# Optimization experiments

Hardware: AMD Instinct MI355X
Metric: run time of the kernel (lower is better)

Reference implementation:

```python
import jax, jax.numpy as jnp
import numpy as np

EPS = 1e-5

def _layernorm(x, gamma):
    # LayerNorm over last dim, no bias (torch LayerNorm(bias=False))
    mu = jnp.mean(x, axis=-1, keepdims=True)
    var = jnp.mean(jnp.square(x - mu), axis=-1, keepdims=True)
    return (x - mu) * jax.lax.rsqrt(var + EPS) * gamma

def setup_inputs() -> dict:
    B, N, D = 32, 1024, 512
    key = jax.random.key(0)
    ks = jax.random.split(key, 6)
    x = jax.random.normal(ks[0], (B, N, D), dtype=jnp.float32)
    # valid lengths in [1, N] so no query row has all keys masked
    belief_base_sizes = jax.random.randint(ks[1], (B,), 1, N + 1, dtype=jnp.int32)
    s = 0.02
    w_qkv = jax.random.normal(ks[2], (D, 3 * D), dtype=jnp.float32) * s
    w_fc = jax.random.normal(ks[3], (D, D), dtype=jnp.float32) * s
    w_proj = jax.random.normal(ks[4], (D, D), dtype=jnp.float32) * s
    g1 = jnp.ones((D,), dtype=jnp.float32)
    g2 = jnp.ones((D,), dtype=jnp.float32)
    return {"x": x, "belief_base_sizes": belief_base_sizes, "g1": g1,
            "w_qkv": w_qkv, "g2": g2, "w_fc": w_fc, "w_proj": w_proj}

def reference(x, belief_base_sizes, g1, w_qkv, g2, w_fc, w_proj):
    B, N, D = x.shape
    h = _layernorm(x, g1)                      # LN1
    qkv = jnp.einsum('bnd,de->bne', h, w_qkv)  # [B,N,3D]
    q, k, v = jnp.split(qkv, 3, axis=-1)
    scores = jnp.einsum('bqd,bkd->bqk', q, k) / jnp.sqrt(jnp.float32(D))
    # mask key columns >= valid size (rows are NOT masked, matching the original)
    col = jnp.arange(N)
    pad = col[None, None, :] >= belief_base_sizes[:, None, None]  # [B,1,N]
    scores = jnp.where(pad, -jnp.inf, scores)
    attn = jax.nn.softmax(scores, axis=-1)
    y = jnp.einsum('bqk,bkd->bqd', attn, v)
    y = _layernorm(y, g2)                      # LN2 (no residual in original)
    y = jnp.einsum('bnd,de->bne', y, w_fc)
    y = jax.nn.gelu(y, approximate=False)      # torch GELU default = exact erf
    y = jnp.einsum('bnd,de->bne', y, w_proj)
    return y
```

## Files before the change

kernel.cpp:

```cpp
#include <hip/hip_runtime.h>
#include <hip/hip_bf16.h>
#include <cmath>


using f16 = _Float16;
typedef _Float16 f16x8 __attribute__((ext_vector_type(8)));
typedef _Float16 f16x4 __attribute__((ext_vector_type(4)));
typedef _Float16 f16x2 __attribute__((ext_vector_type(2)));
typedef float f32x4 __attribute__((ext_vector_type(4)));

#define NB 32
#define NN 1024
#define ND 512

#define GLOAD_LDS16(g, l)                                                     \
    __builtin_amdgcn_global_load_lds(                                         \
        (const __attribute__((address_space(1))) void*)(g),                   \
        (__attribute__((address_space(3))) void*)(l), 16, 0, 0)

__global__ void transpose_cast_all(const float* __restrict__ wqkv, f16* __restrict__ wqkvT,
                                   const float* __restrict__ wfc, f16* __restrict__ wfcT,
                                   const float* __restrict__ wproj, f16* __restrict__ wprojT) {
    const int z = blockIdx.z;
    const float* w = (z == 0) ? wqkv : (z == 1) ? wfc : wproj;
    f16* wT       = (z == 0) ? wqkvT : (z == 1) ? wfcT : wprojT;
    const int Ncols = (z == 0) ? 1536 : 512;
    if ((int)blockIdx.x * 32 >= Ncols) return;

    __shared__ float tile[32][33];
    const int n0 = blockIdx.x * 32, k0 = blockIdx.y * 32;
    const int tx = threadIdx.x, ty = threadIdx.y;
    for (int i = ty; i < 32; i += 8)
        tile[i][tx] = w[(long long)(k0 + i) * Ncols + n0 + tx];
    __syncthreads();
    for (int i = ty; i < 32; i += 8)
        wT[(long long)(n0 + i) * 512 + k0 + tx] = (f16)tile[tx][i];
}

template <typename TIN>
__global__ __launch_bounds__(256) void ln_kernel(const TIN* __restrict__ x,
                                                 const float* __restrict__ gamma,
                                                 f16* __restrict__ out) {
    const int tid = threadIdx.x;
    const long long base = (long long)blockIdx.x * ND;
    float v0, v1;
    if constexpr (sizeof(TIN) == 4) {
        const float2 t = ((const float2*)(x + base))[tid];
        v0 = t.x; v1 = t.y;
    } else {
        const f16x2 t = ((const f16x2*)(x + base))[tid];
        v0 = (float)t.x; v1 = (float)t.y;
    }

    __shared__ float red[8];
    const int wave = tid >> 6, lane = tid & 63;

    float s = v0 + v1;
#pragma unroll
    for (int o = 32; o > 0; o >>= 1) s += __shfl_down(s, o, 64);
    if (lane == 0) red[wave] = s;
    __syncthreads();
    const float mean = (red[0] + red[1] + red[2] + red[3]) * (1.f / 512.f);
    __syncthreads();

    const float d0 = v0 - mean, d1 = v1 - mean;
    float q = d0 * d0 + d1 * d1;
#pragma unroll
    for (int o = 32; o > 0; o >>= 1) q += __shfl_down(q, o, 64);
    if (lane == 0) red[wave] = q;
    __syncthreads();
    const float var = (red[0] + red[1] + red[2] + red[3]) * (1.f / 512.f);
    const float rstd = rsqrtf(var + 1e-5f);

    f16x2 o2;
    o2.x = (f16)(d0 * rstd * gamma[2 * tid]);
    o2.y = (f16)(d1 * rstd * gamma[2 * tid + 1]);
    ((f16x2*)(out + base))[tid] = o2;
}

__global__ __launch_bounds__(256) void softmax_wave(f16* __restrict__ scores,
                                                    const int* __restrict__ sizes) {
    const int b = blockIdx.y;
    const int wave = threadIdx.x >> 6, lane = threadIdx.x & 63;
    const int row = blockIdx.x * 4 + wave;
    f16* srow = scores + ((long long)b * NN + row) * NN;
    const int sz = sizes[b];
    const int keff = (sz + 63) & ~63;
    const int cbase = lane * 16;

    float v[16];
    if (cbase < keff) {
        const f16x8 a0 = *(const f16x8*)&srow[cbase];
        const f16x8 a1 = *(const f16x8*)&srow[cbase + 8];
#pragma unroll
        for (int e = 0; e < 8; e++) { v[e] = (float)a0[e]; v[8 + e] = (float)a1[e]; }
    } else {
#pragma unroll
        for (int e = 0; e < 16; e++) v[e] = 0.f;
    }

    float m = -1e30f;
#pragma unroll
    for (int e = 0; e < 16; e++)
        if (cbase + e < sz) m = fmaxf(m, v[e]);
#pragma unroll
    for (int o = 32; o > 0; o >>= 1) m = fmaxf(m, __shfl_xor(m, o, 64));

    float s = 0.f;
#pragma unroll
    for (int e = 0; e < 16; e++) {
        v[e] = (cbase + e < sz) ? __expf(v[e] - m) : 0.f;
        s += v[e];
    }
#pragma unroll
    for (int o = 32; o > 0; o >>= 1) s += __shfl_xor(s, o, 64);
    const float inv = 1.f / s;

    if (cbase < keff) {
        f16x8 o0, o1;
#pragma unroll
        for (int e = 0; e < 8; e++) {
            o0[e] = (f16)(v[e] * inv);
            o1[e] = (f16)(v[8 + e] * inv);
        }
        *(f16x8*)&srow[cbase] = o0;
        *(f16x8*)&srow[cbase + 8] = o1;
    }
}

__device__ __forceinline__ float gelu_exact(float x) {
    return 0.5f * x * (1.f + erff(x * 0.70710678118654752f));
}

#define STAGE256(t)                                                           \
    { f16* sl = lds + ((t) & 3) * 16384;                                      \
      GLOAD_LDS16(Ap[0] + (t) * 32, sl + tid * 8);                            \
      GLOAD_LDS16(Ap[1] + (t) * 32, sl + (tid + 512) * 8);                    \
      GLOAD_LDS16(Bp[0] + (t) * 32, sl + 8192 + tid * 8);                     \
      GLOAD_LDS16(Bp[1] + (t) * 32, sl + 8192 + (tid + 512) * 8); }

#define COMPUTE256(t)                                                         \
    { const f16* As_ = lds + ((t) & 3) * 16384;                               \
      const f16* Bs_ = As_ + 8192;                                            \
      f16x8 af[8], bf[4];                                                     \
      _Pragma("unroll") for (int i = 0; i < 8; i++)                           \
          af[i] = *(const f16x8*)&As_[(wr + i * 16 + lrow) * 32 + gq];        \
      _Pragma("unroll") for (int j = 0; j < 4; j++)                           \
          bf[j] = *(const f16x8*)&Bs_[(wc + j * 16 + lrow) * 32 + gq];        \
      __builtin_amdgcn_s_setprio(1);                                          \
      _Pragma("unroll") for (int i = 0; i < 8; i++)                           \
      _Pragma("unroll") for (int j = 0; j < 4; j++)                           \
          acc[i][j] = __builtin_amdgcn_mfma_f32_16x16x32_f16(af[i], bf[j], acc[i][j], 0, 0, 0); \
      __builtin_amdgcn_s_setprio(0); }

#define SYNC256(n)                                                            \
    __builtin_amdgcn_sched_barrier(0);                                        \
    asm volatile("s_waitcnt vmcnt(" #n ")" ::: "memory");                     \
    __builtin_amdgcn_s_barrier();                                             \
    asm volatile("" ::: "memory");

template <int MODE>
__global__ __launch_bounds__(512, 2) void gemm256(
    const f16* __restrict__ A, int lda,
    const f16* __restrict__ Bt, int ldb,
    void* __restrict__ Cv, int ldc, void* __restrict__ Cv2) {
    extern __shared__ __align__(16) f16 lds[];

    const int tid = threadIdx.x;
    const int wave = tid >> 6, lane = tid & 63;
    const int wr = (wave >> 2) * 128, wc = (wave & 3) * 64;
    const int lrow = lane & 15, quad = lane >> 4;
    const int gq = (quad ^ ((lrow >> 1) & 3)) * 8;

    const int gx = gridDim.x;
    const int nwg = gx * (int)gridDim.y;
    const int id = blockIdx.y * gx + blockIdx.x;
    const int wid = (id & 7) * (nwg >> 3) + (id >> 3);
    const int m0 = (wid / gx) * 256;
    const int n0 = (wid % gx) * 256;

    f32x4 acc[8][4];
#pragma unroll
    for (int i = 0; i < 8; i++)
#pragma unroll
        for (int j = 0; j < 4; j++) acc[i][j] = (f32x4){0.f, 0.f, 0.f, 0.f};

    const f16* Ap[2];
    const f16* Bp[2];
#pragma unroll
    for (int p = 0; p < 2; p++) {
        const int s = tid + p * 512;
        const int r = s >> 2, g = s & 3;
        const int c = (g ^ ((r >> 1) & 3)) * 8;
        Ap[p] = A + (long long)(m0 + r) * lda + c;
        Bp[p] = Bt + (long long)(n0 + r) * ldb + c;
    }

    STAGE256(0); STAGE256(1); STAGE256(2);

    for (int t = 0; t < 13; ++t) {
        SYNC256(8);
        STAGE256(t + 3);
        COMPUTE256(t);
    }
    SYNC256(8);
    COMPUTE256(13);
    SYNC256(4);
    COMPUTE256(14);
    SYNC256(0);
    COMPUTE256(15);

    const int cbase = n0 + wc + lrow;
    if constexpr (MODE == 3) {
        if (n0 >= 1024) {
            f16* vTp = (f16*)Cv2;
#pragma unroll
            for (int i = 0; i < 8; i++) {
                const int rbase = m0 + wr + i * 16 + quad * 4;
                const int bb = rbase >> 10, nrow = rbase & 1023;
                f16* vb = vTp + (long long)bb * (ND * NN) + nrow;
#pragma unroll
                for (int j = 0; j < 4; j++) {
                    const int col = cbase + j * 16 - 1024;
                    f16x4 pk;
#pragma unroll
                    for (int r = 0; r < 4; r++) pk[r] = (f16)acc[i][j][r];
                    *(f16x4*)&vb[(long long)col * NN] = pk;
                }
            }
            return;
        }
        f16* Ch = (f16*)Cv;
#pragma unroll
        for (int i = 0; i < 8; i++) {
            const int rbase = m0 + wr + i * 16 + quad * 4;
#pragma unroll
            for (int j = 0; j < 4; j++) {
                const int col = cbase + j * 16;
#pragma unroll
                for (int r = 0; r < 4; r++)
                    Ch[(long long)(rbase + r) * ldc + col] = (f16)acc[i][j][r];
            }
        }
        return;
    }
    if constexpr (MODE == 1) {
        float* Cf = (float*)Cv;
#pragma unroll
        for (int i = 0; i < 8; i++) {
            const int rbase = m0 + wr + i * 16 + quad * 4;
#pragma unroll
            for (int j = 0; j < 4; j++) {
                const int col = cbase + j * 16;
#pragma unroll
                for (int r = 0; r < 4; r++)
                    Cf[(long long)(rbase + r) * ldc + col] = acc[i][j][r];
            }
        }
    } else {
        f16* Ch = (f16*)Cv;
#pragma unroll
        for (int i = 0; i < 8; i++) {
            const int rbase = m0 + wr + i * 16 + quad * 4;
#pragma unroll
            for (int j = 0; j < 4; j++) {
                const int col = cbase + j * 16;
#pragma unroll
                for (int r = 0; r < 4; r++)
                    Ch[(long long)(rbase + r) * ldc + col] = (f16)gelu_exact(acc[i][j][r]);
            }
        }
    }
}

template <int MODE, int MASKN, int MASKK>
__global__ __launch_bounds__(256) void gemm_bt(
    const f16* __restrict__ A, int lda, long long strideA,
    const f16* __restrict__ Bt, int ldb, long long strideB,
    void* __restrict__ Cv, int ldc, long long strideC,
    int K, float alpha, const int* __restrict__ sizes, void* __restrict__ Cv2) {
    __shared__ __align__(16) f16 As[128 * 64];
    __shared__ __align__(16) f16 Bs[128 * 64];

    const int tid = threadIdx.x;
    const int wave = tid >> 6, lane = tid & 63;
    const int wr = (wave >> 1) * 64, wc = (wave & 1) * 64;
    const int lrow = lane & 15, quad = lane >> 4;
    const long long m0 = (long long)blockIdx.y * 128;
    const long long n0 = (long long)blockIdx.x * 128;

    if (MASKN) {
        if (n0 >= sizes[blockIdx.z]) return;
    }
    int Keff = K;
    if (MASKK) {
        const int ke = (sizes[blockIdx.z] + 63) & ~63;
        if (ke < Keff) Keff = ke;
    }

    A += (long long)blockIdx.z * strideA;
    Bt += (long long)blockIdx.z * strideB;

    f32x4 acc[4][4];
#pragma unroll
    for (int i = 0; i < 4; i++)
#pragma unroll
        for (int j = 0; j < 4; j++) acc[i][j] = (f32x4){0.f, 0.f, 0.f, 0.f};

    const f16* Ap[4];
    const f16* Bp[4];
#pragma unroll
    for (int p = 0; p < 4; p++) {
        const int s = tid + p * 256;
        const int r = s >> 3, c = ((s & 7) ^ (r & 7)) * 8;
        Ap[p] = A + (m0 + r) * lda + c;
        Bp[p] = Bt + (n0 + r) * ldb + c;
    }

    for (int k0 = 0; k0 < Keff; k0 += 64) {
        __syncthreads();
#pragma unroll
        for (int p = 0; p < 4; p++) GLOAD_LDS16(Ap[p] + k0, &As[(tid + p * 256) * 8]);
#pragma unroll
        for (int p = 0; p < 4; p++) GLOAD_LDS16(Bp[p] + k0, &Bs[(tid + p * 256) * 8]);
        __syncthreads();

#pragma unroll
        for (int h = 0; h < 2; h++) {
            const int gq = ((h * 4 + quad) ^ (lrow & 7)) * 8;
            f16x8 af[4], bf[4];
#pragma unroll
            for (int i = 0; i < 4; i++)
                af[i] = *(const f16x8*)&As[(wr + i * 16 + lrow) * 64 + gq];
#pragma unroll
            for (int j = 0; j < 4; j++)
                bf[j] = *(const f16x8*)&Bs[(wc + j * 16 + lrow) * 64 + gq];
#pragma unroll
            for (int i = 0; i < 4; i++)
#pragma unroll
                for (int j = 0; j < 4; j++)
                    acc[i][j] = __builtin_amdgcn_mfma_f32_16x16x32_f16(af[i], bf[j], acc[i][j], 0, 0, 0);
        }
    }

    f16* Ch = (f16*)Cv + (long long)blockIdx.z * strideC;
#pragma unroll
    for (int i = 0; i < 4; i++) {
        const long long rbase = m0 + wr + i * 16 + quad * 4;
#pragma unroll
        for (int j = 0; j < 4; j++) {
            const long long col = n0 + wc + j * 16 + lrow;
#pragma unroll
            for (int r = 0; r < 4; r++)
                Ch[(rbase + r) * ldc + col] = (f16)(acc[i][j][r] * alpha);
        }
    }
}

extern "C" void kernel_launch(void* const* d_in, const int* in_sizes, int n_in,
                              void* d_out, int out_size, void* d_ws, size_t ws_size,
                              hipStream_t stream) {
    const float* x     = (const float*)d_in[0];
    const int*   sizes = (const int*)d_in[1];
    const float* g1    = (const float*)d_in[2];
    const float* wqkv  = (const float*)d_in[3];
    const float* g2    = (const float*)d_in[4];
    const float* wfc   = (const float*)d_in[5];
    const float* wproj = (const float*)d_in[6];
    float* out = (float*)d_out;
    char* ws = (char*)d_ws;

    f16* wqkvT  = (f16*)(ws + (0ull << 20));
    f16* wfcT   = (f16*)(ws + (2ull << 20));
    f16* wprojT = (f16*)(ws + (3ull << 20));
    f16* qk     = (f16*)(ws + (4ull << 20));
    f16* vT     = (f16*)(ws + (68ull << 20));
    f16* y      = (f16*)(ws + (4ull << 20));
    f16* ln2o   = (f16*)(ws + (36ull << 20));
    f16* gelub  = (f16*)(ws + (68ull << 20));

    f16* h      = (f16*)d_out;
    f16* scores = (f16*)d_out;

    const long long sstr = (long long)NN * NN;
    const long long qstr = (long long)NN * 1024;
    const long long vstr = (long long)ND * NN;
    const long long ystr = (long long)NN * ND;

    const size_t LDSB = 131072;

    transpose_cast_all<<<dim3(48, 16, 3), dim3(32, 8), 0, stream>>>(
        wqkv, wqkvT, wfc, wfcT, wproj, wprojT);

    ln_kernel<float><<<NB * NN, 256, 0, stream>>>(x, g1, h);

    gemm256<3><<<dim3(6, 128), 512, LDSB, stream>>>(
        h, 512, wqkvT, 512, qk, 1024, vT);

    gemm_bt<0, 1, 0><<<dim3(8, 8, 32), 256, 0, stream>>>(
        qk, 1024, qstr, qk + 512, 1024, qstr,
        scores, NN, sstr, 512, 0.044194173824159216f, sizes, nullptr);

    softmax_wave<<<dim3(NN / 4, NB), 256, 0, stream>>>(scores, sizes);

    gemm_bt<0, 0, 1><<<dim3(4, 8, 32), 256, 0, stream>>>(
        scores, NN, sstr, vT, NN, vstr,
        y, ND, ystr, NN, 1.0f, sizes, nullptr);

    ln_kernel<f16><<<NB * NN, 256, 0, stream>>>(y, g2, ln2o);

    gemm256<2><<<dim3(2, 128), 512, LDSB, stream>>>(
        ln2o, 512, wfcT, 512, gelub, 512, nullptr);

    gemm256<1><<<dim3(2, 128), 512, LDSB, stream>>>(
        gelub, 512, wprojT, 512, out, 512, nullptr);
}
```

Baseline: 392.3 us.

## Restructure 256x256 GEMM into ping-pong pipeline with K=64 tiles and quadrant MFMA phases

Replaces the 4-stage K=32 LDS ring in the dense GEMMs with a double-buffered K=64 pipeline. Each iteration is split into four quadrant MFMA phases, and the global-to-LDS loads for the next tiles are interleaved between them with barriers. The LDS swizzle also changes to an 8-way XOR pattern. The aim is finer overlap of loads with MFMA work and fewer sync points per unit of K. The extra barriers and the tighter buffer-reuse ordering add risk of stalls or race-sensitive timing.

```diff
diff --git a/kernel.cpp b/kernel.cpp
--- a/kernel.cpp
+++ b/kernel.cpp
@@ -132,45 +132,19 @@
     return 0.5f * x * (1.f + erff(x * 0.70710678118654752f));
 }
 
-#define STAGE256(t)                                                           \
-    { f16* sl = lds + ((t) & 3) * 16384;                                      \
-      GLOAD_LDS16(Ap[0] + (t) * 32, sl + tid * 8);                            \
-      GLOAD_LDS16(Ap[1] + (t) * 32, sl + (tid + 512) * 8);                    \
-      GLOAD_LDS16(Bp[0] + (t) * 32, sl + 8192 + tid * 8);                     \
-      GLOAD_LDS16(Bp[1] + (t) * 32, sl + 8192 + (tid + 512) * 8); }
-
-#define COMPUTE256(t)                                                         \
-    { const f16* As_ = lds + ((t) & 3) * 16384;                               \
-      const f16* Bs_ = As_ + 8192;                                            \
-      f16x8 af[8], bf[4];                                                     \
-      _Pragma("unroll") for (int i = 0; i < 8; i++)                           \
-          af[i] = *(const f16x8*)&As_[(wr + i * 16 + lrow) * 32 + gq];        \
-      _Pragma("unroll") for (int j = 0; j < 4; j++)                           \
-          bf[j] = *(const f16x8*)&Bs_[(wc + j * 16 + lrow) * 32 + gq];        \
-      __builtin_amdgcn_s_setprio(1);                                          \
-      _Pragma("unroll") for (int i = 0; i < 8; i++)                           \
-      _Pragma("unroll") for (int j = 0; j < 4; j++)                           \
-          acc[i][j] = __builtin_amdgcn_mfma_f32_16x16x32_f16(af[i], bf[j], acc[i][j], 0, 0, 0); \
-      __builtin_amdgcn_s_setprio(0); }
-
-#define SYNC256(n)                                                            \
-    __builtin_amdgcn_sched_barrier(0);                                        \
-    asm volatile("s_waitcnt vmcnt(" #n ")" ::: "memory");                     \
-    __builtin_amdgcn_s_barrier();                                             \
-    asm volatile("" ::: "memory");
+#define SB __builtin_amdgcn_sched_barrier(0)
 
 template <int MODE>
-__global__ __launch_bounds__(512, 2) void gemm256(
+__global__ __launch_bounds__(512, 2) void gemm256p(
     const f16* __restrict__ A, int lda,
     const f16* __restrict__ Bt, int ldb,
-    void* __restrict__ Cv, int ldc, void* __restrict__ Cv2) {
+    void* __restrict__ Cv, int ldc, void* __restrict__ Cv2, int K) {
     extern __shared__ __align__(16) f16 lds[];
 
     const int tid = threadIdx.x;
     const int wave = tid >> 6, lane = tid & 63;
     const int wr = (wave >> 2) * 128, wc = (wave & 3) * 64;
     const int lrow = lane & 15, quad = lane >> 4;
-    const int gq = (quad ^ ((lrow >> 1) & 3)) * 8;
 
     const int gx = gridDim.x;
     const int nwg = gx * (int)gridDim.y;
@@ -179,36 +153,138 @@
     const int m0 = (wid / gx) * 256;
     const int n0 = (wid % gx) * 256;
 
+    const int NT = K >> 6;
+
+    const int srow = tid >> 3;
+    const int scol = ((tid & 7) ^ (srow & 7)) * 8;
+    const f16* sA = A + (long long)(m0 + srow) * lda + scol;
+    const f16* sB = Bt + (long long)(n0 + srow) * ldb + scol;
+
+    auto stgA = [&](int ts, int r0) {
+        GLOAD_LDS16(sA + (long long)r0 * lda + ts * 64,
+                    lds + (ts & 1) * 32768 + r0 * 64 + tid * 8);
+    };
+    auto stgB = [&](int ts, int r0) {
+        GLOAD_LDS16(sB + (long long)r0 * ldb + ts * 64,
+                    lds + (ts & 1) * 32768 + 16384 + r0 * 64 + tid * 8);
+    };
+
     f32x4 acc[8][4];
 #pragma unroll
     for (int i = 0; i < 8; i++)
 #pragma unroll
         for (int j = 0; j < 4; j++) acc[i][j] = (f32x4){0.f, 0.f, 0.f, 0.f};
 
-    const f16* Ap[2];
-    const f16* Bp[2];
-#pragma unroll
-    for (int p = 0; p < 2; p++) {
-        const int s = tid + p * 512;
-        const int r = s >> 2, g = s & 3;
-        const int c = (g ^ ((r >> 1) & 3)) * 8;
-        Ap[p] = A + (long long)(m0 + r) * lda + c;
-        Bp[p] = Bt + (long long)(n0 + r) * ldb + c;
-    }
-
-    STAGE256(0); STAGE256(1); STAGE256(2);
-
-    for (int t = 0; t < 13; ++t) {
-        SYNC256(8);
-        STAGE256(t + 3);
-        COMPUTE256(t);
-    }
-    SYNC256(8);
-    COMPUTE256(13);
-    SYNC256(4);
-    COMPUTE256(14);
-    SYNC256(0);
-    COMPUTE256(15);
+    stgA(0, 0); stgA(0, 64); stgA(0, 128); stgA(0, 192);
+    stgB(0, 0); stgB(0, 64); stgB(0, 128); stgB(0, 192);
+    stgA(1, 0); stgA(1, 64); stgA(1, 128); stgA(1, 192);
+    stgB(1, 0); stgB(1, 64); stgB(1, 128); stgB(1, 192);
+    SB;
+    asm volatile("s_waitcnt vmcnt(8)" ::: "memory");
+    __builtin_amdgcn_s_barrier();
+    SB;
+
+    f16x8 aL[4][2], aH[4][2], bL[2][2], bH[2][2];
+
+    for (int t = 0; t < NT; ++t) {
+        const f16* Ab = lds + (t & 1) * 32768;
+        const f16* Bb = Ab + 16384;
+        const int t1 = (t + 1 < NT) ? t + 1 : t;
+        const int t2 = (t + 2 < NT) ? t + 2 : t;
+
+#pragma unroll
+        for (int i = 0; i < 4; i++)
+#pragma unroll
+            for (int k2 = 0; k2 < 2; k2++)
+                aL[i][k2] = *(const f16x8*)&Ab[(wr + i * 16 + lrow) * 64 +
+                                               (((k2 * 4 + quad) ^ (lrow & 7)) * 8)];
+#pragma unroll
+        for (int j = 0; j < 2; j++)
+#pragma unroll
+            for (int k2 = 0; k2 < 2; k2++)
+                bL[j][k2] = *(const f16x8*)&Bb[(wc + j * 16 + lrow) * 64 +
+                                               (((k2 * 4 + quad) ^ (lrow & 7)) * 8)];
+        stgA(t1, 64); stgA(t1, 192);
+        SB;
+        __builtin_amdgcn_s_barrier();
+        asm volatile("s_waitcnt lgkmcnt(0)" ::: "memory");
+        SB;
+        __builtin_amdgcn_s_setprio(1);
+#pragma unroll
+        for (int i = 0; i < 4; i++)
+#pragma unroll
+            for (int j = 0; j < 2; j++)
+#pragma unroll
+                for (int k2 = 0; k2 < 2; k2++)
+                    acc[i][j] = __builtin_amdgcn_mfma_f32_16x16x32_f16(aL[i][k2], bL[j][k2], acc[i][j], 0, 0, 0);
+        __builtin_amdgcn_s_setprio(0);
+        SB;
+        __builtin_amdgcn_s_barrier();
+
+#pragma unroll
+        for (int j = 0; j < 2; j++)
+#pragma unroll
+            for (int k2 = 0; k2 < 2; k2++)
+                bH[j][k2] = *(const f16x8*)&Bb[(wc + 32 + j * 16 + lrow) * 64 +
+                                               (((k2 * 4 + quad) ^ (lrow & 7)) * 8)];
+        stgA(t2, 0); stgA(t2, 128);
+        SB;
+        __builtin_amdgcn_s_barrier();
+        asm volatile("s_waitcnt lgkmcnt(0)" ::: "memory");
+        SB;
+        __builtin_amdgcn_s_setprio(1);
+#pragma unroll
+        for (int i = 0; i < 4; i++)
+#pragma unroll
+            for (int j = 0; j < 2; j++)
+#pragma unroll
+                for (int k2 = 0; k2 < 2; k2++)
+                    acc[i][2 + j] = __builtin_amdgcn_mfma_f32_16x16x32_f16(aL[i][k2], bH[j][k2], acc[i][2 + j], 0, 0, 0);
+        __builtin_amdgcn_s_setprio(0);
+        SB;
+        __builtin_amdgcn_s_barrier();
+
+#pragma unroll
+        for (int i = 0; i < 4; i++)
+#pragma unroll
+            for (int k2 = 0; k2 < 2; k2++)
+                aH[i][k2] = *(const f16x8*)&Ab[(wr + 64 + i * 16 + lrow) * 64 +
+                                               (((k2 * 4 + quad) ^ (lrow & 7)) * 8)];
+        stgB(t2, 0); stgB(t2, 64);
+        SB;
+        __builtin_amdgcn_s_barrier();
+        asm volatile("s_waitcnt lgkmcnt(0)" ::: "memory");
+        SB;
+        __builtin_amdgcn_s_setprio(1);
+#pragma unroll
+        for (int i = 0; i < 4; i++)
+#pragma unroll
+            for (int j = 0; j < 2; j++)
+#pragma unroll
+                for (int k2 = 0; k2 < 2; k2++)
+                    acc[4 + i][2 + j] = __builtin_amdgcn_mfma_f32_16x16x32_f16(aH[i][k2], bH[j][k2], acc[4 + i][2 + j], 0, 0, 0);
+        __builtin_amdgcn_s_setprio(0);
+        SB;
+        __builtin_amdgcn_s_barrier();
+
+        stgB(t2, 128); stgB(t2, 192);
+        SB;
+        __builtin_amdgcn_s_barrier();
+        SB;
+        __builtin_amdgcn_s_setprio(1);
+#pragma unroll
+        for (int i = 0; i < 4; i++)
+#pragma unroll
+            for (int j = 0; j < 2; j++)
+#pragma unroll
+                for (int k2 = 0; k2 < 2; k2++)
+                    acc[4 + i][j] = __builtin_amdgcn_mfma_f32_16x16x32_f16(aH[i][k2], bL[j][k2], acc[4 + i][j], 0, 0, 0);
+        __builtin_amdgcn_s_setprio(0);
+        SB;
+        asm volatile("s_waitcnt vmcnt(6)" ::: "memory");
+        __builtin_amdgcn_s_barrier();
+        SB;
+    }
 
     const int cbase = n0 + wc + lrow;
     if constexpr (MODE == 3) {
@@ -394,8 +470,8 @@
 
     ln_kernel<float><<<NB * NN, 256, 0, stream>>>(x, g1, h);
 
-    gemm256<3><<<dim3(6, 128), 512, LDSB, stream>>>(
-        h, 512, wqkvT, 512, qk, 1024, vT);
+    gemm256p<3><<<dim3(6, 128), 512, LDSB, stream>>>(
+        h, 512, wqkvT, 512, qk, 1024, vT, 512);
 
     gemm_bt<0, 1, 0><<<dim3(8, 8, 32), 256, 0, stream>>>(
         qk, 1024, qstr, qk + 512, 1024, qstr,
@@ -409,9 +485,9 @@
 
     ln_kernel<f16><<<NB * NN, 256, 0, stream>>>(y, g2, ln2o);
 
-    gemm256<2><<<dim3(2, 128), 512, LDSB, stream>>>(
-        ln2o, 512, wfcT, 512, gelub, 512, nullptr);
-
-    gemm256<1><<<dim3(2, 128), 512, LDSB, stream>>>(
-        gelub, 512, wprojT, 512, out, 512, nullptr);
-}
+    gemm256p<2><<<dim3(2, 128), 512, LDSB, stream>>>(
+        ln2o, 512, wfcT, 512, gelub, 512, nullptr, 512);
+
+    gemm256p<1><<<dim3(2, 128), 512, LDSB, stream>>>(
+        gelub, 512, wprojT, 512, out, 512, nullptr, 512);
+}
```

New measurement: 408.1 us. 4.0% more time.

## Route attention GEMMs through pipelined 256-tile kernel and use wave-per-row LayerNorm

Applied to the files above, without the earlier changes.

Generalizes the 256x256 four-stage pipelined gemm256 kernel with batch strides, alpha scaling, masked N-tile skipping and variable K. It then replaces the simpler 128-tile gemm_bt for the QK^T and PV batched GEMMs. LayerNorm is rewritten to process one row per wave with vectorized loads and shuffle-only reductions, which removes shared memory and block barriers. Larger tiles cut the number of workgroups per batch and the granularity of the key-length masking. They also clamp extra prefetch stages when K is short, which may reduce occupancy or waste some loads.

```diff
diff --git a/kernel.cpp b/kernel.cpp
--- a/kernel.cpp
+++ b/kernel.cpp
@@ -38,44 +38,65 @@
 }
 
 template <typename TIN>
-__global__ __launch_bounds__(256) void ln_kernel(const TIN* __restrict__ x,
-                                                 const float* __restrict__ gamma,
-                                                 f16* __restrict__ out) {
-    const int tid = threadIdx.x;
-    const long long base = (long long)blockIdx.x * ND;
-    float v0, v1;
+__global__ __launch_bounds__(256) void ln_wave(const TIN* __restrict__ x,
+                                               const float* __restrict__ gamma,
+                                               f16* __restrict__ out) {
+    const int wave = threadIdx.x >> 6, lane = threadIdx.x & 63;
+    const long long base = ((long long)blockIdx.x * 4 + wave) * ND;
+
+    float v[8];
+    float g[8];
     if constexpr (sizeof(TIN) == 4) {
-        const float2 t = ((const float2*)(x + base))[tid];
-        v0 = t.x; v1 = t.y;
+        const float4* p = (const float4*)(x + base);
+        const float4 a = p[lane], b = p[lane + 64];
+        v[0] = a.x; v[1] = a.y; v[2] = a.z; v[3] = a.w;
+        v[4] = b.x; v[5] = b.y; v[6] = b.z; v[7] = b.w;
+        const float4* gp = (const float4*)gamma;
+        const float4 ga = gp[lane], gb = gp[lane + 64];
+        g[0] = ga.x; g[1] = ga.y; g[2] = ga.z; g[3] = ga.w;
+        g[4] = gb.x; g[5] = gb.y; g[6] = gb.z; g[7] = gb.w;
     } else {
-        const f16x2 t = ((const f16x2*)(x + base))[tid];
-        v0 = (float)t.x; v1 = (float)t.y;
-    }
-
-    __shared__ float red[8];
-    const int wave = tid >> 6, lane = tid & 63;
-
-    float s = v0 + v1;
-#pragma unroll
-    for (int o = 32; o > 0; o >>= 1) s += __shfl_down(s, o, 64);
-    if (lane == 0) red[wave] = s;
-    __syncthreads();
-    const float mean = (red[0] + red[1] + red[2] + red[3]) * (1.f / 512.f);
-    __syncthreads();
-
-    const float d0 = v0 - mean, d1 = v1 - mean;
-    float q = d0 * d0 + d1 * d1;
-#pragma unroll
-    for (int o = 32; o > 0; o >>= 1) q += __shfl_down(q, o, 64);
-    if (lane == 0) red[wave] = q;
-    __syncthreads();
-    const float var = (red[0] + red[1] + red[2] + red[3]) * (1.f / 512.f);
-    const float rstd = rsqrtf(var + 1e-5f);
-
-    f16x2 o2;
-    o2.x = (f16)(d0 * rstd * gamma[2 * tid]);
-    o2.y = (f16)(d1 * rstd * gamma[2 * tid + 1]);
-    ((f16x2*)(out + base))[tid] = o2;
+        const f16x8 t = ((const f16x8*)(x + base))[lane];
+#pragma unroll
+        for (int e = 0; e < 8; e++) v[e] = (float)t[e];
+        const float4* gp = (const float4*)gamma;
+        const float4 ga = gp[2 * lane], gb = gp[2 * lane + 1];
+        g[0] = ga.x; g[1] = ga.y; g[2] = ga.z; g[3] = ga.w;
+        g[4] = gb.x; g[5] = gb.y; g[6] = gb.z; g[7] = gb.w;
+    }
+
+    float s = 0.f;
+#pragma unroll
+    for (int e = 0; e < 8; e++) s += v[e];
+#pragma unroll
+    for (int o = 32; o > 0; o >>= 1) s += __shfl_xor(s, o, 64);
+    const float mean = s * (1.f / 512.f);
+
+    float q = 0.f;
+#pragma unroll
+    for (int e = 0; e < 8; e++) {
+        v[e] -= mean;
+        q += v[e] * v[e];
+    }
+#pragma unroll
+    for (int o = 32; o > 0; o >>= 1) q += __shfl_xor(q, o, 64);
+    const float rstd = rsqrtf(q * (1.f / 512.f) + 1e-5f);
+
+    if constexpr (sizeof(TIN) == 4) {
+        f16x4 o0, o1;
+#pragma unroll
+        for (int e = 0; e < 4; e++) {
+            o0[e] = (f16)(v[e] * rstd * g[e]);
+            o1[e] = (f16)(v[4 + e] * rstd * g[4 + e]);
+        }
+        ((f16x4*)(out + base))[lane] = o0;
+        ((f16x4*)(out + base))[lane + 64] = o1;
+    } else {
+        f16x8 o8;
+#pragma unroll
+        for (int e = 0; e < 8; e++) o8[e] = (f16)(v[e] * rstd * g[e]);
+        ((f16x8*)(out + base))[lane] = o8;
+    }
 }
 
 __global__ __launch_bounds__(256) void softmax_wave(f16* __restrict__ scores,
@@ -133,11 +154,11 @@
 }
 
 #define STAGE256(t)                                                           \
-    { f16* sl = lds + ((t) & 3) * 16384;                                      \
-      GLOAD_LDS16(Ap[0] + (t) * 32, sl + tid * 8);                            \
-      GLOAD_LDS16(Ap[1] + (t) * 32, sl + (tid + 512) * 8);                    \
-      GLOAD_LDS16(Bp[0] + (t) * 32, sl + 8192 + tid * 8);                     \
-      GLOAD_LDS16(Bp[1] + (t) * 32, sl + 8192 + (tid + 512) * 8); }
+    { const int ts_ = (t); f16* sl = lds + (ts_ & 3) * 16384;                 \
+      GLOAD_LDS16(Ap0 + ts_ * 32, sl + tid * 8);                              \
+      GLOAD_LDS16(Ap1 + ts_ * 32, sl + (tid + 512) * 8);                      \
+      GLOAD_LDS16(Bp0 + ts_ * 32, sl + 8192 + tid * 8);                       \
+      GLOAD_LDS16(Bp1 + ts_ * 32, sl + 8192 + (tid + 512) * 8); }
 
 #define COMPUTE256(t)                                                         \
     { const f16* As_ = lds + ((t) & 3) * 16384;                               \
@@ -159,11 +180,12 @@
     __builtin_amdgcn_s_barrier();                                             \
     asm volatile("" ::: "memory");
 
-template <int MODE>
+template <int MODE, int MASKN, int MASKK>
 __global__ __launch_bounds__(512, 2) void gemm256(
-    const f16* __restrict__ A, int lda,
-    const f16* __restrict__ Bt, int ldb,
-    void* __restrict__ Cv, int ldc, void* __restrict__ Cv2) {
+    const f16* __restrict__ A, int lda, long long strideA,
+    const f16* __restrict__ Bt, int ldb, long long strideB,
+    void* __restrict__ Cv, int ldc, long long strideC,
+    int K, float alpha, const int* __restrict__ sizes, void* __restrict__ Cv2) {
     extern __shared__ __align__(16) f16 lds[];
 
     const int tid = threadIdx.x;
@@ -179,36 +201,44 @@
     const int m0 = (wid / gx) * 256;
     const int n0 = (wid % gx) * 256;
 
+    if (MASKN) {
+        if (n0 >= sizes[blockIdx.z]) return;
+    }
+    int Keff = K;
+    if (MASKK) {
+        const int ke = (sizes[blockIdx.z] + 63) & ~63;
+        if (ke < Keff) Keff = ke;
+    }
+    const int NT = Keff >> 5;
+
+    A += (long long)blockIdx.z * strideA;
+    Bt += (long long)blockIdx.z * strideB;
+
     f32x4 acc[8][4];
 #pragma unroll
     for (int i = 0; i < 8; i++)
 #pragma unroll
         for (int j = 0; j < 4; j++) acc[i][j] = (f32x4){0.f, 0.f, 0.f, 0.f};
 
-    const f16* Ap[2];
-    const f16* Bp[2];
-#pragma unroll
-    for (int p = 0; p < 2; p++) {
-        const int s = tid + p * 512;
-        const int r = s >> 2, g = s & 3;
-        const int c = (g ^ ((r >> 1) & 3)) * 8;
-        Ap[p] = A + (long long)(m0 + r) * lda + c;
-        Bp[p] = Bt + (long long)(n0 + r) * ldb + c;
-    }
-
-    STAGE256(0); STAGE256(1); STAGE256(2);
-
-    for (int t = 0; t < 13; ++t) {
+    const int r0s = tid >> 2, g0s = tid & 3;
+    const int r1s = (tid + 512) >> 2, g1s = tid & 3;
+    const f16* Ap0 = A + (long long)(m0 + r0s) * lda + (g0s ^ ((r0s >> 1) & 3)) * 8;
+    const f16* Ap1 = A + (long long)(m0 + r1s) * lda + (g1s ^ ((r1s >> 1) & 3)) * 8;
+    const f16* Bp0 = Bt + (long long)(n0 + r0s) * ldb + (g0s ^ ((r0s >> 1) & 3)) * 8;
+    const f16* Bp1 = Bt + (long long)(n0 + r1s) * ldb + (g1s ^ ((r1s >> 1) & 3)) * 8;
+
+    const int c1 = (1 < NT - 1) ? 1 : NT - 1;
+    const int c2 = (2 < NT - 1) ? 2 : NT - 1;
+    STAGE256(0); STAGE256(c1); STAGE256(c2);
+
+    for (int t = 0; t < NT; ++t) {
         SYNC256(8);
-        STAGE256(t + 3);
+        const int tn = (t + 3 < NT) ? t + 3 : NT - 1;
+        STAGE256(tn);
         COMPUTE256(t);
     }
-    SYNC256(8);
-    COMPUTE256(13);
-    SYNC256(4);
-    COMPUTE256(14);
-    SYNC256(0);
-    COMPUTE256(15);
+    __builtin_amdgcn_sched_barrier(0);
+    asm volatile("s_waitcnt vmcnt(0)" ::: "memory");
 
     const int cbase = n0 + wc + lrow;
     if constexpr (MODE == 3) {
@@ -245,7 +275,7 @@
         return;
     }
     if constexpr (MODE == 1) {
-        float* Cf = (float*)Cv;
+        float* Cf = (float*)Cv + (long long)blockIdx.z * strideC;
 #pragma unroll
         for (int i = 0; i < 8; i++) {
             const int rbase = m0 + wr + i * 16 + quad * 4;
@@ -257,8 +287,8 @@
                     Cf[(long long)(rbase + r) * ldc + col] = acc[i][j][r];
             }
         }
-    } else {
-        f16* Ch = (f16*)Cv;
+    } else if constexpr (MODE == 2) {
+        f16* Ch = (f16*)Cv + (long long)blockIdx.z * strideC;
 #pragma unroll
         for (int i = 0; i < 8; i++) {
             const int rbase = m0 + wr + i * 16 + quad * 4;
@@ -270,89 +300,18 @@
                     Ch[(long long)(rbase + r) * ldc + col] = (f16)gelu_exact(acc[i][j][r]);
             }
         }
-    }
-}
-
-template <int MODE, int MASKN, int MASKK>
-__global__ __launch_bounds__(256) void gemm_bt(
-    const f16* __restrict__ A, int lda, long long strideA,
-    const f16* __restrict__ Bt, int ldb, long long strideB,
-    void* __restrict__ Cv, int ldc, long long strideC,
-    int K, float alpha, const int* __restrict__ sizes, void* __restrict__ Cv2) {
-    __shared__ __align__(16) f16 As[128 * 64];
-    __shared__ __align__(16) f16 Bs[128 * 64];
-
-    const int tid = threadIdx.x;
-    const int wave = tid >> 6, lane = tid & 63;
-    const int wr = (wave >> 1) * 64, wc = (wave & 1) * 64;
-    const int lrow = lane & 15, quad = lane >> 4;
-    const long long m0 = (long long)blockIdx.y * 128;
-    const long long n0 = (long long)blockIdx.x * 128;
-
-    if (MASKN) {
-        if (n0 >= sizes[blockIdx.z]) return;
-    }
-    int Keff = K;
-    if (MASKK) {
-        const int ke = (sizes[blockIdx.z] + 63) & ~63;
-        if (ke < Keff) Keff = ke;
-    }
-
-    A += (long long)blockIdx.z * strideA;
-    Bt += (long long)blockIdx.z * strideB;
-
-    f32x4 acc[4][4];
-#pragma unroll
-    for (int i = 0; i < 4; i++)
-#pragma unroll
-        for (int j = 0; j < 4; j++) acc[i][j] = (f32x4){0.f, 0.f, 0.f, 0.f};
-
-    const f16* Ap[4];
-    const f16* Bp[4];
-#pragma unroll
-    for (int p = 0; p < 4; p++) {
-        const int s = tid + p * 256;
-        const int r = s >> 3, c = ((s & 7) ^ (r & 7)) * 8;
-        Ap[p] = A + (m0 + r) * lda + c;
-        Bp[p] = Bt + (n0 + r) * ldb + c;
-    }
-
-    for (int k0 = 0; k0 < Keff; k0 += 64) {
-        __syncthreads();
-#pragma unroll
-        for (int p = 0; p < 4; p++) GLOAD_LDS16(Ap[p] + k0, &As[(tid + p * 256) * 8]);
-#pragma unroll
-        for (int p = 0; p < 4; p++) GLOAD_LDS16(Bp[p] + k0, &Bs[(tid + p * 256) * 8]);
-        __syncthreads();
-
-#pragma unroll
-        for (int h = 0; h < 2; h++) {
-            const int gq = ((h * 4 + quad) ^ (lrow & 7)) * 8;
-            f16x8 af[4], bf[4];
-#pragma unroll
-            for (int i = 0; i < 4; i++)
-                af[i] = *(const f16x8*)&As[(wr + i * 16 + lrow) * 64 + gq];
-#pragma unroll
-            for (int j = 0; j < 4; j++)
-                bf[j] = *(const f16x8*)&Bs[(wc + j * 16 + lrow) * 64 + gq];
-#pragma unroll
-            for (int i = 0; i < 4; i++)
-#pragma unroll
-                for (int j = 0; j < 4; j++)
-                    acc[i][j] = __builtin_amdgcn_mfma_f32_16x16x32_f16(af[i], bf[j], acc[i][j], 0, 0, 0);
-        }
-    }
-
-    f16* Ch = (f16*)Cv + (long long)blockIdx.z * strideC;
-#pragma unroll
-    for (int i = 0; i < 4; i++) {
-        const long long rbase = m0 + wr + i * 16 + quad * 4;
-#pragma unroll
-        for (int j = 0; j < 4; j++) {
-            const long long col = n0 + wc + j * 16 + lrow;
-#pragma unroll
-            for (int r = 0; r < 4; r++)
-                Ch[(rbase + r) * ldc + col] = (f16)(acc[i][j][r] * alpha);
+    } else {
+        f16* Ch = (f16*)Cv + (long long)blockIdx.z * strideC;
+#pragma unroll
+        for (int i = 0; i < 8; i++) {
+            const int rbase = m0 + wr + i * 16 + quad * 4;
+#pragma unroll
+            for (int j = 0; j < 4; j++) {
+                const int col = cbase + j * 16;
+#pragma unroll
+                for (int r = 0; r < 4; r++)
+                    Ch[(long long)(rbase + r) * ldc + col] = (f16)(acc[i][j][r] * alpha);
+            }
         }
     }
 }
@@ -392,26 +351,26 @@
     transpose_cast_all<<<dim3(48, 16, 3), dim3(32, 8), 0, stream>>>(
         wqkv, wqkvT, wfc, wfcT, wproj, wprojT);
 
-    ln_kernel<float><<<NB * NN, 256, 0, stream>>>(x, g1, h);
-
-    gemm256<3><<<dim3(6, 128), 512, LDSB, stream>>>(
-        h, 512, wqkvT, 512, qk, 1024, vT);
-
-    gemm_bt<0, 1, 0><<<dim3(8, 8, 32), 256, 0, stream>>>(
+    ln_wave<float><<<NB * NN / 4, 256, 0, stream>>>(x, g1, h);
+
+    gemm256<3, 0, 0><<<dim3(6, 128, 1), 512, LDSB, stream>>>(
+        h, 512, 0, wqkvT, 512, 0, qk, 1024, 0, 512, 1.0f, nullptr, vT);
+
+    gemm256<0, 1, 0><<<dim3(4, 4, 32), 512, LDSB, stream>>>(
         qk, 1024, qstr, qk + 512, 1024, qstr,
         scores, NN, sstr, 512, 0.044194173824159216f, sizes, nullptr);
 
     softmax_wave<<<dim3(NN / 4, NB), 256, 0, stream>>>(scores, sizes);
 
-    gemm_bt<0, 0, 1><<<dim3(4, 8, 32), 256, 0, stream>>>(
+    gemm256<0, 0, 1><<<dim3(2, 4, 32), 512, LDSB, stream>>>(
         scores, NN, sstr, vT, NN, vstr,
         y, ND, ystr, NN, 1.0f, sizes, nullptr);
 
-    ln_kernel<f16><<<NB * NN, 256, 0, stream>>>(y, g2, ln2o);
-
-    gemm256<2><<<dim3(2, 128), 512, LDSB, stream>>>(
-        ln2o, 512, wfcT, 512, gelub, 512, nullptr);
-
-    gemm256<1><<<dim3(2, 128), 512, LDSB, stream>>>(
-        gelub, 512, wprojT, 512, out, 512, nullptr);
-}
+    ln_wave<f16><<<NB * NN / 4, 256, 0, stream>>>(y, g2, ln2o);
+
+    gemm256<2, 0, 0><<<dim3(2, 128, 1), 512, LDSB, stream>>>(
+        ln2o, 512, 0, wfcT, 512, 0, gelub, 512, 0, 512, 1.0f, nullptr, nullptr);
+
+    gemm256<1, 0, 0><<<dim3(2, 128, 1), 512, LDSB, stream>>>(
+        gelub, 512, 0, wprojT, 512, 0, out, 512, 0, 512, 1.0f, nullptr, nullptr);
+}
```

Measured after the change: 377.7 us. 3.7% less time.
